# Kernel optimization log

Measured on AMD Instinct MI355X. Metric: run time of the kernel, lower is better.

Reference implementation:

```python
import jax, jax.numpy as jnp
import numpy as np
from jax import lax

B = 32
ITERS = 100
ALPHA = 0.3  # keras LeakyReLU default alpha
BN_SCALE = np.float32(1.0 / np.sqrt(1.0 + 1e-3))  # inference BN, default moving stats (mean 0, var 1)


def _make_psf_mat():
    # Gaussian PSF mapping 5184 fine (72x72) code positions -> 81 coarse (9x9) pixels, mat shape (5184, 81)
    sigma = (150.0 / 100.0) * 9.0 / 64.0
    coarse = np.arange(9) + 0.5
    fine = (np.arange(72) + 0.5) * 9.0 / 72.0
    g = np.exp(-(fine[:, None] - coarse[None, :]) ** 2 / (2.0 * sigma ** 2))  # (72, 9)
    mat = np.einsum('ia,jb->ijab', g, g).reshape(5184, 81)
    mat = mat / np.linalg.norm(mat, ord=2)  # spectral-normalize so FISTA (mu=1) is stable
    return mat.astype(np.float32)


def leaky(x):
    return jnp.where(x >= 0, x, ALPHA * x)


def conv(x, k, strides=(1, 1)):
    return lax.conv_general_dilated(x, k, strides, 'SAME',
                                    dimension_numbers=('NHWC', 'HWIO', 'NHWC'))


def _forward(inp, mat, w1_k, w1_b, x1_k, x1_b, c51_k, c51_b, c15_k, c15_b,
             c55_k, c55_b, x2_k, x2_b, y17_k, y17_b, y71_k, y71_b, yc_k, yc_b,
             d1_k, d2_k, h1_w, h1_b, h2_w, h2_b, h3_w, h3_b):
    b = inp.shape[0]
    # w branch
    w = leaky(conv(inp, w1_k) + w1_b)  # (B,9,9,1)
    # z branch -> lambda parameter
    z = inp * BN_SCALE
    z = leaky(conv(z, d1_k, strides=(3, 3)) * BN_SCALE)  # (B,3,3,12), downsample: conv no-bias + BN + LeakyReLU
    z = leaky(conv(z, d2_k, strides=(3, 3)) * BN_SCALE)  # (B,1,1,24)
    z = z.reshape(b, -1)
    z = z @ h1_w + h1_b
    z = z @ h2_w + h2_b
    z = z @ h3_w + h3_b  # (B,1)
    param = 0.1 * jax.nn.sigmoid(z)  # (B,1)
    # x branch: normalize (max of |x| over axis 1 only, as in source)
    x = inp / (0.001 + jnp.max(jnp.abs(inp), axis=1, keepdims=True))
    x = leaky(conv(x, x1_k) + x1_b)  # (B,9,9,3)
    # --- CompressedSensing: 100-iter FISTA, vectorized over batch and 3 channels ---
    im = x.reshape(b, 81, 3).transpose(0, 2, 1)  # (B,3,81) row-major flatten per channel
    lam = (param * 0.1)[:, :, None]  # (B,1,1), mu = 1.0

    def step(carry, _):
        y_tmp, y_last, t = carry
        resid = im - jnp.einsum('bcn,nk->bck', y_tmp, mat)      # (B,3,81)  = im - mat^T y
        re = jnp.einsum('bck,nk->bcn', resid, mat)              # (B,3,5184) = mat (im - mat^T y)
        wv = y_tmp + re
        y_new = jax.nn.relu(wv - lam) - jax.nn.relu(-wv - lam)  # soft threshold
        t_n = (1.0 + jnp.sqrt(1.0 + 4.0 * t * t)) / 2.0
        y_next = y_new + (t - 1.0) / t_n * (y_new - y_last)
        return (y_next, y_new, t_n), None

    init = (jnp.zeros((b, 3, 5184), jnp.float32),
            jnp.zeros((b, 3, 5184), jnp.float32),
            jnp.float32(1.0))
    (_, y_new, _), _ = lax.scan(step, init, None, length=ITERS)
    cs_out = y_new.transpose(0, 2, 1).reshape(b, 72, 72, 3)  # stack channels last then reshape
    x = conv(cs_out, c51_k, strides=(2, 2)) + c51_b   # (B,36,36,16), no activation
    x = conv(x, c15_k, strides=(2, 2)) + c15_b        # (B,18,18,32)
    x = conv(x, c55_k, strides=(2, 2)) + c55_b        # (B,9,9,64)
    x = leaky(conv(x, x2_k) + x2_b)                   # (B,9,9,8)
    # y branch
    y1 = conv(inp, y17_k) + y17_b                     # (B,9,9,32)
    y2 = conv(inp, y71_k) + y71_b                     # (B,9,9,32)
    y = leaky(conv(jnp.concatenate([y1, y2], axis=-1), yc_k) + yc_b)  # (B,9,9,32)
    out = jnp.concatenate([w, x, y], axis=-1)         # (B,9,9,41)
    return out, cs_out


def setup_inputs() -> dict:
    key = jax.random.key(0)
    ks = jax.random.split(key, 20)
    rn = lambda k, s, sc=0.1: sc * jax.random.normal(k, s, dtype=jnp.float32)
    x1_k = jnp.clip(1.0 + 0.3 * jax.random.normal(ks[1], (1, 1, 3, 3)), 0.0, None).astype(jnp.float32)
    return {
        'inp': jax.random.normal(ks[0], (B, 9, 9, 3), dtype=jnp.float32),
        'mat': jnp.asarray(_make_psf_mat()),
        'w1_k': rn(ks[2], (1, 1, 3, 1)), 'w1_b': jnp.zeros((1,), jnp.float32),
        'x1_k': x1_k, 'x1_b': jnp.zeros((3,), jnp.float32),
        'c51_k': rn(ks[3], (5, 1, 3, 16)), 'c51_b': jnp.zeros((16,), jnp.float32),
        'c15_k': rn(ks[4], (1, 5, 16, 32)), 'c15_b': jnp.zeros((32,), jnp.float32),
        'c55_k': rn(ks[5], (5, 5, 32, 64)), 'c55_b': jnp.zeros((64,), jnp.float32),
        'x2_k': rn(ks[6], (1, 1, 64, 8)), 'x2_b': jnp.zeros((8,), jnp.float32),
        'y17_k': rn(ks[7], (1, 7, 3, 32)), 'y17_b': jnp.zeros((32,), jnp.float32),
        'y71_k': rn(ks[8], (7, 1, 3, 32)), 'y71_b': jnp.zeros((32,), jnp.float32),
        'yc_k': rn(ks[9], (1, 1, 64, 32)), 'yc_b': jnp.zeros((32,), jnp.float32),
        'd1_k': rn(ks[10], (5, 5, 3, 12)), 'd2_k': rn(ks[11], (5, 5, 12, 24)),
        'h1_w': rn(ks[12], (24, 24), 0.2), 'h1_b': jnp.zeros((24,), jnp.float32),
        'h2_w': rn(ks[13], (24, 12), 0.2), 'h2_b': jnp.zeros((12,), jnp.float32),
        'h3_w': rn(ks[14], (12, 1), 0.2), 'h3_b': jnp.zeros((1,), jnp.float32),
    }


def reference(inp, mat, w1_k, w1_b, x1_k, x1_b, c51_k, c51_b, c15_k, c15_b,
              c55_k, c55_b, x2_k, x2_b, y17_k, y17_b, y71_k, y71_b, yc_k, yc_b,
              d1_k, d2_k, h1_w, h1_b, h2_w, h2_b, h3_w, h3_b):
    return _forward(inp, mat, w1_k, w1_b, x1_k, x1_b, c51_k, c51_b, c15_k, c15_b,
                    c55_k, c55_b, x2_k, x2_b, y17_k, y17_b, y71_k, y71_b, yc_k, yc_b,
                    d1_k, d2_k, h1_w, h1_b, h2_w, h2_b, h3_w, h3_b)
```

## Files before the change

### kernel.cpp

```cpp
#include <hip/hip_runtime.h>
#include <math.h>

#define LEAKY(x) ((x) >= 0.f ? (x) : 0.3f*(x))

#define G_OFF   0
#define IM_OFF  648
#define LAM_OFF 8424
#define WB_OFF  8456
#define YBR_OFF 11048
#define X1_OFF  93992
#define X2_OFF  757544
#define X3_OFF  1089320

#define OUT0 106272

__global__ __launch_bounds__(256) void prep_kernel(
    const float* __restrict__ inp, const float* __restrict__ mat,
    const float* __restrict__ w1_k, const float* __restrict__ w1_b,
    const float* __restrict__ x1_k, const float* __restrict__ x1_b,
    const float* __restrict__ y17_k, const float* __restrict__ y17_b,
    const float* __restrict__ y71_k, const float* __restrict__ y71_b,
    const float* __restrict__ yc_k, const float* __restrict__ yc_b,
    const float* __restrict__ d1_k, const float* __restrict__ d2_k,
    const float* __restrict__ h1_w, const float* __restrict__ h1_b,
    const float* __restrict__ h2_w, const float* __restrict__ h2_b,
    const float* __restrict__ h3_w, const float* __restrict__ h3_b,
    float* __restrict__ ws)
{
    int t = threadIdx.x;
    if (blockIdx.x == 0) {
        float rs = rsqrtf(mat[0]);
        for (int u = t; u < 648; u += 256) {
            int i = u / 9, a = u % 9;
            ws[G_OFF + u] = mat[(size_t)(i*72)*81 + a*9] * rs;
        }
        return;
    }
    int b = blockIdx.x - 1;
    __shared__ float sin_[243];
    __shared__ float cm[27];
    __shared__ float cat[5184];
    __shared__ float z1[108];
    __shared__ float z2[24];
    __shared__ float v1[24];
    __shared__ float v2[12];

    const float BN  = 1.0f / sqrtf(1.001f);
    const float BN2 = BN * BN;

    for (int u = t; u < 243; u += 256) sin_[u] = inp[b*243 + u];
    __syncthreads();

    if (t < 81) {
        float s = w1_b[0];
        for (int i = 0; i < 3; ++i) s += sin_[t*3+i] * w1_k[i];
        ws[WB_OFF + b*81 + t] = LEAKY(s);
    } else if (t < 108) {
        int u = t - 81;
        float m = 0.f;
        for (int r = 0; r < 9; ++r) m = fmaxf(m, fabsf(sin_[r*27 + u]));
        cm[u] = 0.001f + m;
    }
    if (t >= 128 && t < 236) {
        int u = t - 128;
        int o = u % 12, ox = (u/12) % 3, oy = u/36;
        float s = 0.f;
        for (int kh = 0; kh < 5; ++kh) {
            int iy = oy*3 - 1 + kh;
            if (iy < 0 || iy > 8) continue;
            for (int kw = 0; kw < 5; ++kw) {
                int ix = ox*3 - 1 + kw;
                if (ix < 0 || ix > 8) continue;
                for (int i = 0; i < 3; ++i)
                    s += sin_[(iy*9+ix)*3 + i] * d1_k[((kh*5+kw)*3 + i)*12 + o];
            }
        }
        z1[u] = LEAKY(BN2 * s);
    }
    __syncthreads();

    if (t < 243) {
        int o = t / 81, p = t % 81;
        int c = p % 9;
        float s = x1_b[o];
        for (int i = 0; i < 3; ++i)
            s += (sin_[p*3+i] / cm[c*3+i]) * x1_k[i*3 + o];
        ws[IM_OFF + (b*3 + o)*81 + p] = LEAKY(s);
    }
    __syncthreads();

    if (t < 24) {
        float s = 0.f;
        for (int kh = 1; kh < 4; ++kh)
            for (int kw = 1; kw < 4; ++kw)
                for (int i = 0; i < 12; ++i)
                    s += z1[((kh-1)*3 + (kw-1))*12 + i] * d2_k[((kh*5+kw)*12 + i)*24 + t];
        z2[t] = LEAKY(BN * s);
    }
    __syncthreads();
    if (t < 24) {
        float s = h1_b[t];
        for (int i = 0; i < 24; ++i) s += z2[i] * h1_w[i*24 + t];
        v1[t] = s;
    }
    __syncthreads();
    if (t < 12) {
        float s = h2_b[t];
        for (int i = 0; i < 24; ++i) s += v1[i] * h2_w[i*12 + t];
        v2[t] = s;
    }
    __syncthreads();
    if (t == 0) {
        float s = h3_b[0];
        for (int i = 0; i < 12; ++i) s += v2[i] * h3_w[i];
        ws[LAM_OFF + b] = 0.01f / (1.f + expf(-s));
    }

    for (int u = t; u < 5184; u += 256) {
        int pos = u / 64, i = u % 64;
        int r = pos / 9, c = pos % 9;
        float s;
        if (i < 32) {
            s = y17_b[i];
            for (int kw = 0; kw < 7; ++kw) {
                int cc = c - 3 + kw;
                if (cc < 0 || cc > 8) continue;
                for (int ii = 0; ii < 3; ++ii)
                    s += sin_[(r*9+cc)*3 + ii] * y17_k[(kw*3+ii)*32 + i];
            }
        } else {
            int i2 = i - 32;
            s = y71_b[i2];
            for (int kh = 0; kh < 7; ++kh) {
                int rr = r - 3 + kh;
                if (rr < 0 || rr > 8) continue;
                for (int ii = 0; ii < 3; ++ii)
                    s += sin_[(rr*9+c)*3 + ii] * y71_k[(kh*3+ii)*32 + i2];
            }
        }
        cat[pos*64 + i] = s;
    }
    __syncthreads();
    for (int u = t; u < 2592; u += 256) {
        int pos = u / 32, o = u % 32;
        float s = yc_b[o];
        for (int i = 0; i < 64; ++i) s += cat[pos*64 + i] * yc_k[i*32 + o];
        ws[YBR_OFF + (b*81 + pos)*32 + o] = LEAKY(s);
    }
}


#define DPP_XOR1 0xB1
#define DPP_XOR2 0x4E
#define DPP_HM   0x141
#define DPP_ROR8 0x128

template<int CTRL>
__device__ __forceinline__ float dppadd(float v) {
    return v + __int_as_float(__builtin_amdgcn_update_dpp(
        0, __float_as_int(v), CTRL, 0xF, 0xF, true));
}

#define STEPMID(s,sm,sp) { \
    float re = gm*q##sm + g0*q##s + gp*q##sp; \
    float wv = Yv##s + re; \
    float cl = fminf(fmaxf(wv, -lam), lam); \
    float yn = wv - cl; \
    float yx = yn + cmom*(yn - Yl##s); \
    Yl##s = yn; Yv##s = yx; \
    u##sm += yx*gm; u##s += yx*g0; u##sp += yx*gp; }
#define STEP0 { \
    float re = g0*q0 + gp*q1; \
    float wv = Yv0 + re; \
    float cl = fminf(fmaxf(wv, -lam), lam); \
    float yn = wv - cl; \
    float yx = yn + cmom*(yn - Yl0); \
    Yl0 = yn; Yv0 = yx; \
    u0 += yx*g0; u1 += yx*gp; }
#define STEP8 { \
    float re = gm*q7 + g0*q8; \
    float wv = Yv8 + re; \
    float cl = fminf(fmaxf(wv, -lam), lam); \
    float yn = wv - cl; \
    float yx = yn + cmom*(yn - Yl8); \
    Yl8 = yn; Yv8 = yx; \
    u7 += yx*gm; u8 += yx*g0; }

#define TSP(a) { float v = u##a; \
    v = dppadd<DPP_XOR1>(v); v = dppadd<DPP_XOR2>(v); v = dppadd<DPP_HM>(v); \
    float vA = v*Gjg, vB = v*Gj8; \
    spA_##a = dppadd<DPP_ROR8>(vA); spB_##a = dppadd<DPP_ROR8>(vB); }

#define QT3(a) float q##a = cmc*rm_##a + c0c*r0_##a + cpc*rp_##a;

#define OUTW(s) cs_out[(size_t)(b*5184 + (8*s+gg)*72 + j)*3 + ch] = Yl##s;

__global__ __launch_bounds__(576, 3) void fista_kernel(
    const float* __restrict__ ws, float* __restrict__ cs_out)
{
    __shared__ __align__(16) float SPm[36*108];
    __shared__ __align__(16) float Rm[108];

    int t = threadIdx.x;
    int b = blockIdx.x / 3, ch = blockIdx.x % 3;
    const float* g = ws + G_OFF;
    float lam = ws[LAM_OFF + b];

    int j = t >> 3, gg = t & 7;
    int l = t & 63;
    int w = t >> 6;
    int rr = j & 7;

    float gm = g[(gg + 8)*9 + 0];
    float g0 = g[gg*9 + 0];
    float gp = g[gg*9 + 1];

    float cmc = (w > 0) ? g[(rr + 8)*9 + 0] : 0.f;
    float c0c = g[rr*9 + 0];
    float cpc = (w < 8) ? g[rr*9 + 1] : 0.f;
    int bmr = (w > 0) ? w - 1 : 0;
    int bpr = (w < 8) ? w + 1 : 8;

    float Gjg = g[j*9 + gg];
    float Gj8 = g[j*9 + 8];

    int ab = t >> 2, pp = t & 3;
    int aa = ab / 9, bb = ab % 9;
    float im_ab = (t < 324) ? ws[IM_OFF + (b*3 + ch)*81 + ab] : 0.f;

    if (t < 81) {
        Rm[(t % 9)*12 + (t / 9)] = ws[IM_OFF + (b*3 + ch)*81 + t];
    }

    float Yv0=0,Yv1=0,Yv2=0,Yv3=0,Yv4=0,Yv5=0,Yv6=0,Yv7=0,Yv8=0;
    float Yl0=0,Yl1=0,Yl2=0,Yl3=0,Yl4=0,Yl5=0,Yl6=0,Yl7=0,Yl8=0;
    float tk = 1.f;
    __syncthreads();

    for (int it = 0; it < 100; ++it) {
        float tn = 0.5f*(1.f + sqrtf(1.f + 4.f*tk*tk));
        float cmom = (tk - 1.f) / tn;
        tk = tn;

        float4 mv0 = *(const float4*)(Rm + bmr*12);
        float4 mv1 = *(const float4*)(Rm + bmr*12 + 4);
        float  mv2 = Rm[bmr*12 + 8];
        float rm_0=mv0.x, rm_1=mv0.y, rm_2=mv0.z, rm_3=mv0.w,
              rm_4=mv1.x, rm_5=mv1.y, rm_6=mv1.z, rm_7=mv1.w, rm_8=mv2;
        float4 zv0 = *(const float4*)(Rm + w*12);
        float4 zv1 = *(const float4*)(Rm + w*12 + 4);
        float  zv2 = Rm[w*12 + 8];
        float r0_0=zv0.x, r0_1=zv0.y, r0_2=zv0.z, r0_3=zv0.w,
              r0_4=zv1.x, r0_5=zv1.y, r0_6=zv1.z, r0_7=zv1.w, r0_8=zv2;
        float4 pv0 = *(const float4*)(Rm + bpr*12);
        float4 pv1 = *(const float4*)(Rm + bpr*12 + 4);
        float  pv2 = Rm[bpr*12 + 8];
        float rp_0=pv0.x, rp_1=pv0.y, rp_2=pv0.z, rp_3=pv0.w,
              rp_4=pv1.x, rp_5=pv1.y, rp_6=pv1.z, rp_7=pv1.w, rp_8=pv2;
        QT3(0) QT3(1) QT3(2) QT3(3) QT3(4) QT3(5) QT3(6) QT3(7) QT3(8)

        float u0=0,u1=0,u2=0,u3=0,u4=0,u5=0,u6=0,u7=0,u8=0;
        STEP0
        STEPMID(1,0,2) STEPMID(2,1,3) STEPMID(3,2,4) STEPMID(4,3,5)
        STEPMID(5,4,6) STEPMID(6,5,7) STEPMID(7,6,8)
        STEP8
        if (it == 99) break;

        float spA_0,spA_1,spA_2,spA_3,spA_4,spA_5,spA_6,spA_7,spA_8;
        float spB_0,spB_1,spB_2,spB_3,spB_4,spB_5,spB_6,spB_7,spB_8;
        TSP(0) TSP(1) TSP(2) TSP(3) TSP(4) TSP(5) TSP(6) TSP(7) TSP(8)

        int setb = ((t >> 6)*4 + (l >> 4))*108;
        if ((l & 8) == 0) {
            float* d = &SPm[setb + gg*12];
            ((float4*)d)[0] = make_float4(spA_0,spA_1,spA_2,spA_3);
            ((float4*)d)[1] = make_float4(spA_4,spA_5,spA_6,spA_7);
            d[8] = spA_8;
            if (gg == 0) {
                float* d2 = &SPm[setb + 96];
                ((float4*)d2)[0] = make_float4(spB_0,spB_1,spB_2,spB_3);
                ((float4*)d2)[1] = make_float4(spB_4,spB_5,spB_6,spB_7);
                d2[8] = spB_8;
            }
        }
        __syncthreads();

        if (t < 324) {
            float s = SPm[(bb*4 + pp)*108 + bb*12 + aa];
            if (bb > 0) s += SPm[((bb-1)*4 + pp)*108 + bb*12 + aa];
            if (bb < 8) s += SPm[((bb+1)*4 + pp)*108 + bb*12 + aa];
            s = dppadd<DPP_XOR1>(s);
            s = dppadd<DPP_XOR2>(s);
            if (pp == 0) Rm[bb*12 + aa] = im_ab - s;
        }
        __syncthreads();
    }

    OUTW(0) OUTW(1) OUTW(2) OUTW(3) OUTW(4) OUTW(5) OUTW(6) OUTW(7) OUTW(8)
}

__global__ __launch_bounds__(256) void c51_kernel(
    const float* __restrict__ cs, const float* __restrict__ k,
    const float* __restrict__ bias, float* __restrict__ out)
{
    int id = blockIdx.x*256 + threadIdx.x;
    if (id >= 32*36*36*16) return;
    int o = id & 15; int rest = id >> 4;
    int ox = rest % 36; rest /= 36; int oy = rest % 36; int b = rest / 36;
    float s = bias[o];
    int ix = ox*2;
    for (int kh = 0; kh < 5; ++kh) {
        int iy = oy*2 - 1 + kh;
        if (iy < 0 || iy >= 72) continue;
        const float* p = cs + ((size_t)(b*72 + iy)*72 + ix)*3;
        const float* kk = k + kh*48 + o;
        s += p[0]*kk[0] + p[1]*kk[16] + p[2]*kk[32];
    }
    out[id] = s;
}

__global__ __launch_bounds__(256) void c15_kernel(
    const float* __restrict__ x1, const float* __restrict__ k,
    const float* __restrict__ bias, float* __restrict__ out)
{
    int id = blockIdx.x*256 + threadIdx.x;
    if (id >= 32*18*18*32) return;
    int o = id & 31; int rest = id >> 5;
    int ox = rest % 18; rest /= 18; int oy = rest % 18; int b = rest / 18;
    float s = bias[o];
    int iy = oy*2;
    for (int kw = 0; kw < 5; ++kw) {
        int ix = ox*2 - 1 + kw;
        if (ix < 0 || ix >= 36) continue;
        const float* p = x1 + ((size_t)(b*36 + iy)*36 + ix)*16;
        const float* kk = k + kw*512 + o;
        for (int i = 0; i < 16; ++i) s += p[i]*kk[i*32];
    }
    out[id] = s;
}

__global__ __launch_bounds__(256) void c55_kernel(
    const float* __restrict__ x2, const float* __restrict__ k,
    const float* __restrict__ bias, float* __restrict__ out)
{
    int id = blockIdx.x*256 + threadIdx.x;
    if (id >= 32*9*9*64) return;
    int o = id & 63; int rest = id >> 6;
    int ox = rest % 9; rest /= 9; int oy = rest % 9; int b = rest / 9;
    float s = bias[o];
    for (int kh = 0; kh < 5; ++kh) {
        int iy = oy*2 - 1 + kh;
        if (iy < 0 || iy >= 18) continue;
        for (int kw = 0; kw < 5; ++kw) {
            int ix = ox*2 - 1 + kw;
            if (ix < 0 || ix >= 18) continue;
            const float* p = x2 + ((size_t)(b*18 + iy)*18 + ix)*32;
            const float* kk = k + (kh*5+kw)*2048 + o;
            for (int i = 0; i < 32; ++i) s += p[i]*kk[i*64];
        }
    }
    out[id] = s;
}

__global__ __launch_bounds__(256) void out_kernel(
    const float* __restrict__ ws, const float* __restrict__ x2_k,
    const float* __restrict__ x2_b, float* __restrict__ out)
{
    int id = blockIdx.x*256 + threadIdx.x;
    if (id >= OUT0) return;
    int q = id % 41; int rest = id / 41;
    int cc = rest % 9; rest /= 9; int r = rest % 9; int b = rest / 9;
    float val;
    if (q == 0) {
        val = ws[WB_OFF + b*81 + r*9 + cc];
    } else if (q <= 8) {
        int o = q - 1;
        const float* p = ws + X3_OFF + ((size_t)(b*9 + r)*9 + cc)*64;
        float s = x2_b[o];
        for (int i = 0; i < 64; ++i) s += p[i]*x2_k[i*8 + o];
        val = LEAKY(s);
    } else {
        val = ws[YBR_OFF + ((size_t)(b*81 + r*9 + cc))*32 + (q - 9)];
    }
    out[id] = val;
}

extern "C" void kernel_launch(void* const* d_in, const int* in_sizes, int n_in,
                              void* d_out, int out_size, void* d_ws, size_t ws_size,
                              hipStream_t stream) {
    const float* inp   = (const float*)d_in[0];
    const float* mat   = (const float*)d_in[1];
    const float* w1_k  = (const float*)d_in[2];
    const float* w1_b  = (const float*)d_in[3];
    const float* x1_k  = (const float*)d_in[4];
    const float* x1_b  = (const float*)d_in[5];
    const float* c51_k = (const float*)d_in[6];
    const float* c51_b = (const float*)d_in[7];
    const float* c15_k = (const float*)d_in[8];
    const float* c15_b = (const float*)d_in[9];
    const float* c55_k = (const float*)d_in[10];
    const float* c55_b = (const float*)d_in[11];
    const float* x2_k  = (const float*)d_in[12];
    const float* x2_b  = (const float*)d_in[13];
    const float* y17_k = (const float*)d_in[14];
    const float* y17_b = (const float*)d_in[15];
    const float* y71_k = (const float*)d_in[16];
    const float* y71_b = (const float*)d_in[17];
    const float* yc_k  = (const float*)d_in[18];
    const float* yc_b  = (const float*)d_in[19];
    const float* d1_k  = (const float*)d_in[20];
    const float* d2_k  = (const float*)d_in[21];
    const float* h1_w  = (const float*)d_in[22];
    const float* h1_b  = (const float*)d_in[23];
    const float* h2_w  = (const float*)d_in[24];
    const float* h2_b  = (const float*)d_in[25];
    const float* h3_w  = (const float*)d_in[26];
    const float* h3_b  = (const float*)d_in[27];

    float* ws  = (float*)d_ws;
    float* out = (float*)d_out;
    float* cs  = out + OUT0;

    hipLaunchKernelGGL(prep_kernel, dim3(33), dim3(256), 0, stream,
        inp, mat, w1_k, w1_b, x1_k, x1_b, y17_k, y17_b, y71_k, y71_b,
        yc_k, yc_b, d1_k, d2_k, h1_w, h1_b, h2_w, h2_b, h3_w, h3_b, ws);
    hipLaunchKernelGGL(fista_kernel, dim3(96), dim3(576), 0, stream, ws, cs);
    hipLaunchKernelGGL(c51_kernel, dim3(2592), dim3(256), 0, stream, cs, c51_k, c51_b, ws + X1_OFF);
    hipLaunchKernelGGL(c15_kernel, dim3(1296), dim3(256), 0, stream, ws + X1_OFF, c15_k, c15_b, ws + X2_OFF);
    hipLaunchKernelGGL(c55_kernel, dim3(648), dim3(256), 0, stream, ws + X2_OFF, c55_k, c55_b, ws + X3_OFF);
    hipLaunchKernelGGL(out_kernel, dim3(416), dim3(256), 0, stream, ws, x2_k, x2_b, out);
}
```

Before: 351.2 us.

## Fuse c51+c15 convs per batch in LDS and c55 with output kernel

Merges the c51 and c15 convolutions into one kernel with one 1024-thread block per batch item. The intermediate 36x36x16 activation stays in shared memory instead of making a round trip through global memory. It also fuses the c55 convolution with the final output assembly, so the 1x1 x2 projection reads c55 results from shared memory. This removes two launches and two intermediate global buffers, but the first fused kernel runs only 32 blocks, which leaves most of the GPU idle.

```diff
diff --git a/kernel.cpp b/kernel.cpp
--- a/kernel.cpp
+++ b/kernel.cpp
@@ -8,9 +8,7 @@
 #define LAM_OFF 8424
 #define WB_OFF  8456
 #define YBR_OFF 11048
-#define X1_OFF  93992
 #define X2_OFF  757544
-#define X3_OFF  1089320
 
 #define OUT0 106272
 
@@ -299,90 +297,95 @@
     OUTW(0) OUTW(1) OUTW(2) OUTW(3) OUTW(4) OUTW(5) OUTW(6) OUTW(7) OUTW(8)
 }
 
-__global__ __launch_bounds__(256) void c51_kernel(
-    const float* __restrict__ cs, const float* __restrict__ k,
-    const float* __restrict__ bias, float* __restrict__ out)
+__global__ __launch_bounds__(1024) void c51c15_kernel(
+    const float* __restrict__ cs, const float* __restrict__ k51,
+    const float* __restrict__ b51, const float* __restrict__ k15,
+    const float* __restrict__ b15, float* __restrict__ x2out)
 {
-    int id = blockIdx.x*256 + threadIdx.x;
-    if (id >= 32*36*36*16) return;
-    int o = id & 15; int rest = id >> 4;
-    int ox = rest % 36; rest /= 36; int oy = rest % 36; int b = rest / 36;
-    float s = bias[o];
-    int ix = ox*2;
-    for (int kh = 0; kh < 5; ++kh) {
-        int iy = oy*2 - 1 + kh;
-        if (iy < 0 || iy >= 72) continue;
-        const float* p = cs + ((size_t)(b*72 + iy)*72 + ix)*3;
-        const float* kk = k + kh*48 + o;
-        s += p[0]*kk[0] + p[1]*kk[16] + p[2]*kk[32];
-    }
-    out[id] = s;
-}
-
-__global__ __launch_bounds__(256) void c15_kernel(
-    const float* __restrict__ x1, const float* __restrict__ k,
-    const float* __restrict__ bias, float* __restrict__ out)
-{
-    int id = blockIdx.x*256 + threadIdx.x;
-    if (id >= 32*18*18*32) return;
-    int o = id & 31; int rest = id >> 5;
-    int ox = rest % 18; rest /= 18; int oy = rest % 18; int b = rest / 18;
-    float s = bias[o];
-    int iy = oy*2;
-    for (int kw = 0; kw < 5; ++kw) {
-        int ix = ox*2 - 1 + kw;
-        if (ix < 0 || ix >= 36) continue;
-        const float* p = x1 + ((size_t)(b*36 + iy)*36 + ix)*16;
-        const float* kk = k + kw*512 + o;
-        for (int i = 0; i < 16; ++i) s += p[i]*kk[i*32];
-    }
-    out[id] = s;
-}
-
-__global__ __launch_bounds__(256) void c55_kernel(
-    const float* __restrict__ x2, const float* __restrict__ k,
-    const float* __restrict__ bias, float* __restrict__ out)
-{
-    int id = blockIdx.x*256 + threadIdx.x;
-    if (id >= 32*9*9*64) return;
-    int o = id & 63; int rest = id >> 6;
-    int ox = rest % 9; rest /= 9; int oy = rest % 9; int b = rest / 9;
-    float s = bias[o];
-    for (int kh = 0; kh < 5; ++kh) {
-        int iy = oy*2 - 1 + kh;
-        if (iy < 0 || iy >= 18) continue;
+    __shared__ float x1s[36*36*16];
+    int t = threadIdx.x;
+    int b = blockIdx.x;
+
+    for (int u = t; u < 36*36*16; u += 1024) {
+        int o = u & 15; int rest = u >> 4;
+        int ox = rest % 36; int oy = rest / 36;
+        float s = b51[o];
+        int ix = ox*2;
+        for (int kh = 0; kh < 5; ++kh) {
+            int iy = oy*2 - 1 + kh;
+            if (iy < 0 || iy >= 72) continue;
+            const float* p = cs + ((size_t)(b*72 + iy)*72 + ix)*3;
+            const float* kk = k51 + kh*48 + o;
+            s += p[0]*kk[0] + p[1]*kk[16] + p[2]*kk[32];
+        }
+        x1s[u] = s;
+    }
+    __syncthreads();
+
+    for (int u = t; u < 18*18*32; u += 1024) {
+        int o = u & 31; int rest = u >> 5;
+        int ox = rest % 18; int oy = rest / 18;
+        float s = b15[o];
+        int iy = oy*2;
         for (int kw = 0; kw < 5; ++kw) {
             int ix = ox*2 - 1 + kw;
-            if (ix < 0 || ix >= 18) continue;
-            const float* p = x2 + ((size_t)(b*18 + iy)*18 + ix)*32;
-            const float* kk = k + (kh*5+kw)*2048 + o;
-            for (int i = 0; i < 32; ++i) s += p[i]*kk[i*64];
-        }
-    }
-    out[id] = s;
-}
-
-__global__ __launch_bounds__(256) void out_kernel(
-    const float* __restrict__ ws, const float* __restrict__ x2_k,
-    const float* __restrict__ x2_b, float* __restrict__ out)
+            if (ix < 0 || ix >= 36) continue;
+            const float* p = x1s + ((iy*36) + ix)*16;
+            const float* kk = k15 + kw*512 + o;
+            for (int i = 0; i < 16; ++i) s += p[i]*kk[i*32];
+        }
+        x2out[((size_t)(b*18 + oy)*18 + ox)*32 + o] = s;
+    }
+}
+
+__global__ __launch_bounds__(256) void c55out_kernel(
+    const float* __restrict__ x2g, const float* __restrict__ k55,
+    const float* __restrict__ b55, const float* __restrict__ ws,
+    const float* __restrict__ x2_k, const float* __restrict__ x2_b,
+    float* __restrict__ out)
 {
-    int id = blockIdx.x*256 + threadIdx.x;
-    if (id >= OUT0) return;
-    int q = id % 41; int rest = id / 41;
-    int cc = rest % 9; rest /= 9; int r = rest % 9; int b = rest / 9;
-    float val;
-    if (q == 0) {
-        val = ws[WB_OFF + b*81 + r*9 + cc];
-    } else if (q <= 8) {
-        int o = q - 1;
-        const float* p = ws + X3_OFF + ((size_t)(b*9 + r)*9 + cc)*64;
-        float s = x2_b[o];
-        for (int i = 0; i < 64; ++i) s += p[i]*x2_k[i*8 + o];
-        val = LEAKY(s);
-    } else {
-        val = ws[YBR_OFF + ((size_t)(b*81 + r*9 + cc))*32 + (q - 9)];
-    }
-    out[id] = val;
+    __shared__ float x3s[4][64];
+    int t = threadIdx.x;
+    int lp = t >> 6;
+    int o  = t & 63;
+    int pg = blockIdx.x*4 + lp;
+    int b  = pg / 81, rc = pg % 81;
+    int r  = rc / 9,  c  = rc % 9;
+
+    {
+        float s = b55[o];
+        for (int kh = 0; kh < 5; ++kh) {
+            int iy = r*2 - 1 + kh;
+            if (iy < 0 || iy >= 18) continue;
+            for (int kw = 0; kw < 5; ++kw) {
+                int ix = c*2 - 1 + kw;
+                if (ix < 0 || ix >= 18) continue;
+                const float* p = x2g + ((size_t)(b*18 + iy)*18 + ix)*32;
+                const float* kk = k55 + (kh*5+kw)*2048 + o;
+                for (int i = 0; i < 32; ++i) s += p[i]*kk[i*64];
+            }
+        }
+        x3s[lp][o] = s;
+    }
+    __syncthreads();
+
+    if (t < 4*41) {
+        int lp2 = t / 41, q = t % 41;
+        int pg2 = blockIdx.x*4 + lp2;
+        int b2  = pg2 / 81, rc2 = pg2 % 81;
+        float val;
+        if (q == 0) {
+            val = ws[WB_OFF + b2*81 + rc2];
+        } else if (q <= 8) {
+            int o2 = q - 1;
+            float s = x2_b[o2];
+            for (int i = 0; i < 64; ++i) s += x3s[lp2][i]*x2_k[i*8 + o2];
+            val = LEAKY(s);
+        } else {
+            val = ws[YBR_OFF + (size_t)(b2*81 + rc2)*32 + (q - 9)];
+        }
+        out[(size_t)pg2*41 + q] = val;
+    }
 }
 
 extern "C" void kernel_launch(void* const* d_in, const int* in_sizes, int n_in,
@@ -425,8 +428,8 @@
         inp, mat, w1_k, w1_b, x1_k, x1_b, y17_k, y17_b, y71_k, y71_b,
         yc_k, yc_b, d1_k, d2_k, h1_w, h1_b, h2_w, h2_b, h3_w, h3_b, ws);
     hipLaunchKernelGGL(fista_kernel, dim3(96), dim3(576), 0, stream, ws, cs);
-    hipLaunchKernelGGL(c51_kernel, dim3(2592), dim3(256), 0, stream, cs, c51_k, c51_b, ws + X1_OFF);
-    hipLaunchKernelGGL(c15_kernel, dim3(1296), dim3(256), 0, stream, ws + X1_OFF, c15_k, c15_b, ws + X2_OFF);
-    hipLaunchKernelGGL(c55_kernel, dim3(648), dim3(256), 0, stream, ws + X2_OFF, c55_k, c55_b, ws + X3_OFF);
-    hipLaunchKernelGGL(out_kernel, dim3(416), dim3(256), 0, stream, ws, x2_k, x2_b, out);
-}
+    hipLaunchKernelGGL(c51c15_kernel, dim3(32), dim3(1024), 0, stream,
+        cs, c51_k, c51_b, c15_k, c15_b, ws + X2_OFF);
+    hipLaunchKernelGGL(c55out_kernel, dim3(648), dim3(256), 0, stream,
+        ws + X2_OFF, c55_k, c55_b, ws, x2_k, x2_b, out);
+}
```

New measurement: 384.9 us. 1.1x slower.
